# Performance work log

Hardware: AMD Instinct MI355X
Metric: run time of the kernel (lower is better)

Reference implementation:

```python
import jax, jax.numpy as jnp
import numpy as np

N = 100000      # nodes
E = 1600000     # random edges (self-loops appended, as PyG GATConv does)
IN = 128        # in_channels
HID = 8         # hidden_channels per head
HEADS = 8
OUT = 40        # out_channels (classes)
NEG_SLOPE = 0.2 # PyG GATConv default


def _xavier(k, shape, fan_in, fan_out):
    lim = np.sqrt(6.0 / (fan_in + fan_out)).astype(np.float32)
    return jax.random.uniform(k, shape, jnp.float32, -lim, lim)


def setup_inputs() -> dict:
    key = jax.random.key(0)
    ks = jax.random.split(key, 8)
    x = jax.random.normal(ks[0], (N, IN), jnp.float32)
    ei = jax.random.randint(ks[1], (2, E), 0, N)
    loops = jnp.arange(N)
    edge_index = jnp.concatenate([ei, jnp.stack([loops, loops])], axis=1)  # [2, E+N]
    W1 = _xavier(ks[2], (HEADS * HID, IN), IN, HEADS * HID)
    att_src1 = _xavier(ks[3], (HEADS, HID), HID, 1)
    att_dst1 = _xavier(ks[4], (HEADS, HID), HID, 1)
    b1 = jnp.zeros((HEADS * HID,), jnp.float32)
    W2 = _xavier(ks[5], (OUT, HEADS * HID), HEADS * HID, OUT)
    att_src2 = _xavier(ks[6], (1, OUT), OUT, 1)
    att_dst2 = _xavier(ks[7], (1, OUT), OUT, 1)
    b2 = jnp.zeros((OUT,), jnp.float32)
    return {"x": x, "edge_index": edge_index, "W1": W1, "att_src1": att_src1,
            "att_dst1": att_dst1, "b1": b1, "W2": W2, "att_src2": att_src2,
            "att_dst2": att_dst2, "b2": b2}


def _gat_conv(x, src, dst, W, a_src, a_dst, b, heads, ch, concat):
    n = x.shape[0]
    h = (x @ W.T).reshape(n, heads, ch)                       # [N,H,C]
    a_s = jnp.sum(h * a_src[None], axis=-1)                   # [N,H]
    a_d = jnp.sum(h * a_dst[None], axis=-1)                   # [N,H]
    e = jax.nn.leaky_relu(a_s[src] + a_d[dst], NEG_SLOPE)     # [Eall,H]
    # segment softmax over edges sharing a destination node
    e_max = jax.ops.segment_max(e, dst, num_segments=n)
    ex = jnp.exp(e - e_max[dst])
    denom = jax.ops.segment_sum(ex, dst, num_segments=n)
    alpha = ex / denom[dst]                                   # [Eall,H]
    msg = h[src] * alpha[:, :, None]                          # [Eall,H,C]
    out = jax.ops.segment_sum(msg, dst, num_segments=n)       # [N,H,C]
    out = out.reshape(n, heads * ch) if concat else out.mean(axis=1)
    return out + b


def reference(x, edge_index, W1, att_src1, att_dst1, b1, W2, att_src2, att_dst2, b2):
    # eval mode: dropout is identity
    src, dst = edge_index[0], edge_index[1]
    h = _gat_conv(x, src, dst, W1, att_src1, att_dst1, b1, HEADS, HID, True)
    h = jax.nn.elu(h)
    out = _gat_conv(h, src, dst, W2, att_src2, att_dst2, b2, 1, OUT, False)
    return out
```

## Files before the change

### kernel.cpp

```cpp
#include <hip/hip_runtime.h>
#include <hip/hip_bf16.h>

#define IN_CH   128
#define HID     8
#define HEADS   8
#define C1      64
#define OUT_CH  40
#define NEG     0.2f
#define NPART   8

__device__ __forceinline__ float b2f(unsigned short u) {
    return __uint_as_float(((unsigned int)u) << 16);
}
__device__ __forceinline__ float blo(unsigned int p) { return __uint_as_float(p << 16); }
__device__ __forceinline__ float bhi(unsigned int p) { return __uint_as_float(p & 0xffff0000u); }
__device__ __forceinline__ unsigned short f2b(float f) {
    unsigned int u = __float_as_uint(f);
    unsigned int r = (u + 0x7fffu + ((u >> 16) & 1u)) >> 16;
    return (unsigned short)r;
}
__device__ __forceinline__ float lrelu(float v) { return v > 0.f ? v : NEG * v; }

#define P_W1    0
#define P_AS1   8192
#define P_AD1   8256
#define P_B1    8320
#define P_W2    8384
#define P_AS2   10944
#define P_AD2   10984
#define P_B2    11024
#define P_TOT   11064

__global__ __launch_bounds__(256) void k0_detect(
        const unsigned int* __restrict__ x32,
        const void* W1, const void* as1, const void* ad1, const void* b1,
        const void* W2, const void* as2, const void* ad2, const void* b2,
        int* __restrict__ flag, float* __restrict__ pf) {
    int t = threadIdx.x;
    __shared__ int sflag;
    if (t < 64) {
        unsigned int lo = x32[t] & 0xffffu;
        int ex = (int)((lo >> 7) & 0xff);
        bool sane = (ex >= 112 && ex <= 143);
        unsigned long long m = __ballot(sane);
        if (t == 0) {
            int isbf = (__popcll(m) >= 32) ? 1 : 0;
            sflag = isbf;
            *flag = isbf;
        }
    }
    __syncthreads();
    const int isbf = sflag;
#define CONV(dstoff, srcp, cnt)                                         \
    if (isbf) {                                                         \
        const unsigned short* sp = (const unsigned short*)(srcp);       \
        for (int i = t; i < (cnt); i += 256) pf[(dstoff) + i] = b2f(sp[i]); \
    } else {                                                            \
        const float* sp = (const float*)(srcp);                         \
        for (int i = t; i < (cnt); i += 256) pf[(dstoff) + i] = sp[i];  \
    }
    CONV(P_W1,  W1, 8192)
    CONV(P_AS1, as1, 64)
    CONV(P_AD1, ad1, 64)
    CONV(P_B1,  b1, 64)
    CONV(P_W2,  W2, 2560)
    CONV(P_AS2, as2, 40)
    CONV(P_AD2, ad2, 40)
    CONV(P_B2,  b2, 40)
#undef CONV
}

__global__ __launch_bounds__(256) void kA_hist(
        const int* __restrict__ dst, int* __restrict__ deg,
        int e_all, int n_nodes) {
    int part = blockIdx.x & (NPART - 1);
    int nm   = gridDim.x >> 3;
    int mblk = blockIdx.x >> 3;
    int lo = (int)((long long)part * n_nodes / NPART);
    int hi = (int)((long long)(part + 1) * n_nodes / NPART);
    for (int e = mblk * 256 + threadIdx.x; e < e_all; e += nm * 256) {
        int d = dst[e];
        if (d >= lo && d < hi) atomicAdd(&deg[d], 1);
    }
}

__global__ __launch_bounds__(256) void kB1_scan(
        const int* __restrict__ deg, int* __restrict__ offs,
        int* __restrict__ bsum, int n) {
    __shared__ int sd[256];
    int t = threadIdx.x;
    int i = blockIdx.x * 256 + t;
    int v = (i < n) ? deg[i] : 0;
    sd[t] = v;
    __syncthreads();
    for (int off = 1; off < 256; off <<= 1) {
        int u = (t >= off) ? sd[t - off] : 0;
        __syncthreads();
        sd[t] += u;
        __syncthreads();
    }
    if (i < n) offs[i] = sd[t] - v;
    if (t == 255) bsum[blockIdx.x] = sd[255];
}

__global__ __launch_bounds__(512) void kB2_scanb(
        const int* __restrict__ bsum, int* __restrict__ bsumx, int nb) {
    __shared__ int sd[512];
    int t = threadIdx.x;
    int v = (t < nb) ? bsum[t] : 0;
    sd[t] = v;
    __syncthreads();
    for (int off = 1; off < 512; off <<= 1) {
        int u = (t >= off) ? sd[t - off] : 0;
        __syncthreads();
        sd[t] += u;
        __syncthreads();
    }
    if (t < nb) bsumx[t] = sd[t] - v;
}

__global__ __launch_bounds__(256) void kB3_fix(
        int* __restrict__ offs, const int* __restrict__ bsumx,
        int* __restrict__ cursor, int n) {
    int i = blockIdx.x * 256 + threadIdx.x;
    if (i >= n) return;
    int o = offs[i] + bsumx[blockIdx.x];
    offs[i] = o;
    cursor[i] = o;
}

__global__ __launch_bounds__(256) void kC_scatter(
        const int* __restrict__ src, const int* __restrict__ dst,
        int* __restrict__ cursor, int* __restrict__ csr_src,
        int e_all, int n_nodes) {
    int part = blockIdx.x & (NPART - 1);
    int nm   = gridDim.x >> 3;
    int mblk = blockIdx.x >> 3;
    int lo = (int)((long long)part * n_nodes / NPART);
    int hi = (int)((long long)(part + 1) * n_nodes / NPART);
    for (int e = mblk * 256 + threadIdx.x; e < e_all; e += nm * 256) {
        int d = dst[e];
        if (d >= lo && d < hi) {
            int pos = atomicAdd(&cursor[d], 1);
            csr_src[pos] = src[e];
        }
    }
}

__global__ __launch_bounds__(256) void k1_gemm1(
        const void* __restrict__ x, const float* __restrict__ pf,
        const int* __restrict__ flagp,
        unsigned short* __restrict__ h1b, float* __restrict__ as1, float* __restrict__ ad1,
        int n_nodes) {
    int tid = threadIdx.x;
    int w = tid >> 6, t = tid & 63;
    const int isbf = *flagp;
    __shared__ float wTf[8192];
    __shared__ float xsf[4 * IN_CH];
    for (int e = tid; e < 8192; e += 256) {
        int row = e >> 7, k = e & 127;
        int g = k >> 2, j = k & 3;
        wTf[(g * 64 + ((row + g) & 63)) * 4 + j] = pf[P_W1 + e];
    }
    __syncthreads();
    const float4* wT4 = (const float4*)wTf;
    int base = blockIdx.x * 32 + w * 8;
    for (int i = 0; i < 8; ++i) {
        int n = base + i;
        bool ok = (n < n_nodes);
        if (ok) {
            if (isbf) {
                unsigned int p = ((const unsigned int*)x)[(size_t)n * 64 + t];
                xsf[w * IN_CH + 2 * t]     = blo(p);
                xsf[w * IN_CH + 2 * t + 1] = bhi(p);
            } else {
                float2 f = ((const float2*)x)[(size_t)n * 64 + t];
                xsf[w * IN_CH + 2 * t]     = f.x;
                xsf[w * IN_CH + 2 * t + 1] = f.y;
            }
        }
        __syncthreads();
        if (ok) {
            const float4* xv = (const float4*)(xsf + w * IN_CH);
            float acc = 0.f;
#pragma unroll
            for (int g = 0; g < 32; ++g) {
                float4 wv = wT4[g * 64 + ((t + g) & 63)];
                float4 x4 = xv[g];
                acc += x4.x * wv.x + x4.y * wv.y + x4.z * wv.z + x4.w * wv.w;
            }
            h1b[(size_t)n * C1 + t] = f2b(acc);
            float as = acc * pf[P_AS1 + t];
            float ad = acc * pf[P_AD1 + t];
            for (int off = 1; off < 8; off <<= 1) {
                as += __shfl_xor(as, off, 64);
                ad += __shfl_xor(ad, off, 64);
            }
            if ((t & 7) == 0) {
                as1[(size_t)n * HEADS + (t >> 3)] = as;
                ad1[(size_t)n * HEADS + (t >> 3)] = ad;
            }
        }
        __syncthreads();
    }
}

__global__ __launch_bounds__(256) void k3_fused1(
        const int* __restrict__ offs, const int* __restrict__ deg,
        const int* __restrict__ csr_src,
        const float* __restrict__ as1, const float* __restrict__ ad1,
        const unsigned short* __restrict__ h1b, const float* __restrict__ pf,
        unsigned short* __restrict__ x2, int n_nodes) {
    int d = blockIdx.x * 4 + (threadIdx.x >> 6);
    if (d >= n_nodes) return;
    int t = threadIdx.x & 63;
    int head = t >> 3;
    float adv = ad1[(size_t)d * HEADS + head];
    int start = offs[d];
    int dg = deg[d];
    float acc = 0.f, den = 0.f;
    int j = 0;
    for (; j + 4 <= dg; j += 4) {
        int s0 = csr_src[start + j];
        int s1 = csr_src[start + j + 1];
        int s2 = csr_src[start + j + 2];
        int s3 = csr_src[start + j + 3];
        float v0 = as1[(size_t)s0 * HEADS + head] + adv;
        float v1 = as1[(size_t)s1 * HEADS + head] + adv;
        float v2 = as1[(size_t)s2 * HEADS + head] + adv;
        float v3 = as1[(size_t)s3 * HEADS + head] + adv;
        float h0 = b2f(h1b[(size_t)s0 * C1 + t]);
        float h1 = b2f(h1b[(size_t)s1 * C1 + t]);
        float h2 = b2f(h1b[(size_t)s2 * C1 + t]);
        float h3 = b2f(h1b[(size_t)s3 * C1 + t]);
        float e0 = __expf(lrelu(v0));
        float e1 = __expf(lrelu(v1));
        float e2 = __expf(lrelu(v2));
        float e3 = __expf(lrelu(v3));
        den += (e0 + e1) + (e2 + e3);
        acc += (e0 * h0 + e1 * h1) + (e2 * h2 + e3 * h3);
    }
    for (; j < dg; ++j) {
        int s = csr_src[start + j];
        float v = as1[(size_t)s * HEADS + head] + adv;
        float e = __expf(lrelu(v));
        den += e;
        acc += e * b2f(h1b[(size_t)s * C1 + t]);
    }
    float o = acc / den + pf[P_B1 + t];
    o = o > 0.f ? o : (__expf(o) - 1.f);
    x2[(size_t)d * C1 + t] = f2b(o);
}

__global__ __launch_bounds__(256) void k4_gemm2(
        const unsigned short* __restrict__ x2, const float* __restrict__ pf,
        unsigned short* __restrict__ h2b, float* __restrict__ as2, float* __restrict__ ad2,
        int n_nodes) {
    int tid = threadIdx.x;
    int w = tid >> 6, t = tid & 63;
    __shared__ float wTf[4096];
    __shared__ float xsf[4 * C1];
    for (int e = tid; e < 2560; e += 256) {
        int row = e >> 6, k = e & 63;
        int g = k >> 2, j = k & 3;
        wTf[(g * 64 + ((row + g) & 63)) * 4 + j] = pf[P_W2 + e];
    }
    __syncthreads();
    const float4* wT4 = (const float4*)wTf;
    int base = blockIdx.x * 32 + w * 8;
    for (int i = 0; i < 8; ++i) {
        int n = base + i;
        bool ok = (n < n_nodes);
        if (ok && t < 32) {
            unsigned int p = ((const unsigned int*)x2)[(size_t)n * 32 + t];
            xsf[w * C1 + 2 * t]     = blo(p);
            xsf[w * C1 + 2 * t + 1] = bhi(p);
        }
        __syncthreads();
        if (ok) {
            float hs = 0.f, hd = 0.f;
            if (t < OUT_CH) {
                const float4* xv = (const float4*)(xsf + w * C1);
                float acc = 0.f;
#pragma unroll
                for (int g = 0; g < 16; ++g) {
                    float4 wv = wT4[g * 64 + ((t + g) & 63)];
                    float4 x4 = xv[g];
                    acc += x4.x * wv.x + x4.y * wv.y + x4.z * wv.z + x4.w * wv.w;
                }
                h2b[(size_t)n * OUT_CH + t] = f2b(acc);
                hs = acc * pf[P_AS2 + t];
                hd = acc * pf[P_AD2 + t];
            }
            for (int off = 1; off < 64; off <<= 1) {
                hs += __shfl_xor(hs, off, 64);
                hd += __shfl_xor(hd, off, 64);
            }
            if (t == 0) { as2[n] = hs; ad2[n] = hd; }
        }
        __syncthreads();
    }
}

__global__ __launch_bounds__(256) void k6_fused2(
        const int* __restrict__ offs, const int* __restrict__ deg,
        const int* __restrict__ csr_src,
        const float* __restrict__ as2, const float* __restrict__ ad2,
        const unsigned short* __restrict__ h2b, const float* __restrict__ pf,
        const int* __restrict__ flagp, void* __restrict__ outp, int n_nodes) {
    int d = blockIdx.x * 4 + (threadIdx.x >> 6);
    if (d >= n_nodes) return;
    int t = threadIdx.x & 63;
    float adv = ad2[d];
    int start = offs[d];
    int dg = deg[d];
    bool act = (t < OUT_CH);
    int tc = act ? t : 0;
    float acc = 0.f, den = 0.f;
    int j = 0;
    for (; j + 4 <= dg; j += 4) {
        int s0 = csr_src[start + j];
        int s1 = csr_src[start + j + 1];
        int s2 = csr_src[start + j + 2];
        int s3 = csr_src[start + j + 3];
        float v0 = as2[s0] + adv;
        float v1 = as2[s1] + adv;
        float v2 = as2[s2] + adv;
        float v3 = as2[s3] + adv;
        float h0 = b2f(h2b[(size_t)s0 * OUT_CH + tc]);
        float h1 = b2f(h2b[(size_t)s1 * OUT_CH + tc]);
        float h2 = b2f(h2b[(size_t)s2 * OUT_CH + tc]);
        float h3 = b2f(h2b[(size_t)s3 * OUT_CH + tc]);
        float e0 = __expf(lrelu(v0));
        float e1 = __expf(lrelu(v1));
        float e2 = __expf(lrelu(v2));
        float e3 = __expf(lrelu(v3));
        den += (e0 + e1) + (e2 + e3);
        acc += (e0 * h0 + e1 * h1) + (e2 * h2 + e3 * h3);
    }
    for (; j < dg; ++j) {
        int s = csr_src[start + j];
        float v = as2[s] + adv;
        float e = __expf(lrelu(v));
        den += e;
        acc += e * b2f(h2b[(size_t)s * OUT_CH + tc]);
    }
    if (!act) return;
    float o = acc / den + pf[P_B2 + t];
    size_t idx = (size_t)d * OUT_CH + t;
    if (*flagp) ((unsigned short*)outp)[idx] = f2b(o);
    else        ((float*)outp)[idx] = o;
}

extern "C" void kernel_launch(void* const* d_in, const int* in_sizes, int n_in,
                              void* d_out, int out_size, void* d_ws, size_t ws_size,
                              hipStream_t stream) {
    const void* x  = d_in[0];
    const int*  ei = (const int*)d_in[1];

    const int n_nodes = in_sizes[0] / IN_CH;
    const int e_all   = in_sizes[1] / 2;
    const int* srcI = ei;
    const int* dstI = ei + e_all;

    float* ws = (float*)d_ws;
    const size_t n = (size_t)n_nodes;
    int* deg     = (int*)ws;
    int* offs    = deg + n;
    int* cursor  = offs + n;
    int* bsum    = cursor + n;
    int* bsumx   = bsum + 512;
    int* csr_src = bsumx + 512;
    float* A     = ws + 3 * n + 1024 + (size_t)e_all;
    float* as1   = A;
    float* ad1   = A + 8 * n;
    unsigned short* h1b = (unsigned short*)(A + 16 * n);
    unsigned short* x2  = (unsigned short*)(A + 48 * n);
    int*   flagp = (int*)(A + 80 * n);
    float* pf    = A + 80 * n + 16;
    float* as2 = as1;
    float* ad2 = ad1;
    unsigned short* h2b = h1b;

    k0_detect<<<1, 256, 0, stream>>>((const unsigned int*)x,
        d_in[2], d_in[3], d_in[4], d_in[5], d_in[6], d_in[7], d_in[8], d_in[9],
        flagp, pf);

    hipMemsetAsync(deg, 0, n * sizeof(int), stream);

    kA_hist<<<1024, 256, 0, stream>>>(dstI, deg, e_all, n_nodes);

    int nb = (n_nodes + 255) / 256;
    kB1_scan<<<nb, 256, 0, stream>>>(deg, offs, bsum, n_nodes);
    kB2_scanb<<<1, 512, 0, stream>>>(bsum, bsumx, nb);
    kB3_fix<<<nb, 256, 0, stream>>>(offs, bsumx, cursor, n_nodes);

    kC_scatter<<<1024, 256, 0, stream>>>(srcI, dstI, cursor, csr_src, e_all, n_nodes);

    int gb = (n_nodes + 31) / 32;
    k1_gemm1<<<gb, 256, 0, stream>>>(x, pf, flagp, h1b, as1, ad1, n_nodes);

    k3_fused1<<<(n_nodes + 3) / 4, 256, 0, stream>>>(offs, deg, csr_src, as1, ad1, h1b, pf, x2, n_nodes);

    k4_gemm2<<<gb, 256, 0, stream>>>(x2, pf, h2b, as2, ad2, n_nodes);

    k6_fused2<<<(n_nodes + 3) / 4, 256, 0, stream>>>(offs, deg, csr_src, as2, ad2, h2b, pf, flagp, d_out, n_nodes);
}
```

Before: 545.1 us.

## Replace first-layer scalar GEMM with bf16 MFMA kernel

The first linear projection (x @ W1.T) now runs on matrix cores through 16x16x32 bf16 MFMA instructions instead of a shared-memory scalar FP32 dot-product loop. W1 is converted to bf16 once in the setup kernel, and each wave loads its W1 fragments straight from global memory. Each wave handles 16 nodes with no block-level syncs, and the attention logits are reduced with shuffles. When x arrives as fp32 it is rounded to bf16 before the multiply, which lowers the precision of the first layer's GEMM inputs.

```diff
diff --git a/kernel.cpp b/kernel.cpp
--- a/kernel.cpp
+++ b/kernel.cpp
@@ -8,6 +8,9 @@
 #define OUT_CH  40
 #define NEG     0.2f
 #define NPART   8
+
+typedef __attribute__((ext_vector_type(8))) short  short8;
+typedef __attribute__((ext_vector_type(4))) float  f32x4;
 
 __device__ __forceinline__ float b2f(unsigned short u) {
     return __uint_as_float(((unsigned int)u) << 16);
@@ -35,7 +38,8 @@
         const unsigned int* __restrict__ x32,
         const void* W1, const void* as1, const void* ad1, const void* b1,
         const void* W2, const void* as2, const void* ad2, const void* b2,
-        int* __restrict__ flag, float* __restrict__ pf) {
+        int* __restrict__ flag, float* __restrict__ pf,
+        unsigned short* __restrict__ w1bf) {
     int t = threadIdx.x;
     __shared__ int sflag;
     if (t < 64) {
@@ -68,6 +72,13 @@
     CONV(P_AD2, ad2, 40)
     CONV(P_B2,  b2, 40)
 #undef CONV
+    if (isbf) {
+        const unsigned short* sp = (const unsigned short*)W1;
+        for (int i = t; i < 8192; i += 256) w1bf[i] = sp[i];
+    } else {
+        const float* sp = (const float*)W1;
+        for (int i = t; i < 8192; i += 256) w1bf[i] = f2b(sp[i]);
+    }
 }
 
 __global__ __launch_bounds__(256) void kA_hist(
@@ -147,61 +158,71 @@
     }
 }
 
-__global__ __launch_bounds__(256) void k1_gemm1(
-        const void* __restrict__ x, const float* __restrict__ pf,
-        const int* __restrict__ flagp,
+__global__ __launch_bounds__(256) void k1_mfma(
+        const void* __restrict__ x, const unsigned short* __restrict__ w1bf,
+        const float* __restrict__ pf, const int* __restrict__ flagp,
         unsigned short* __restrict__ h1b, float* __restrict__ as1, float* __restrict__ ad1,
         int n_nodes) {
     int tid = threadIdx.x;
-    int w = tid >> 6, t = tid & 63;
+    int wv = tid >> 6, L = tid & 63;
+    int m = L & 15, q = L >> 4;
+    int base = blockIdx.x * 64 + wv * 16;
+    if (base >= n_nodes) return;
     const int isbf = *flagp;
-    __shared__ float wTf[8192];
-    __shared__ float xsf[4 * IN_CH];
-    for (int e = tid; e < 8192; e += 256) {
-        int row = e >> 7, k = e & 127;
-        int g = k >> 2, j = k & 3;
-        wTf[(g * 64 + ((row + g) & 63)) * 4 + j] = pf[P_W1 + e];
-    }
-    __syncthreads();
-    const float4* wT4 = (const float4*)wTf;
-    int base = blockIdx.x * 32 + w * 8;
-    for (int i = 0; i < 8; ++i) {
-        int n = base + i;
-        bool ok = (n < n_nodes);
-        if (ok) {
-            if (isbf) {
-                unsigned int p = ((const unsigned int*)x)[(size_t)n * 64 + t];
-                xsf[w * IN_CH + 2 * t]     = blo(p);
-                xsf[w * IN_CH + 2 * t + 1] = bhi(p);
-            } else {
-                float2 f = ((const float2*)x)[(size_t)n * 64 + t];
-                xsf[w * IN_CH + 2 * t]     = f.x;
-                xsf[w * IN_CH + 2 * t + 1] = f.y;
+
+    short8 bfr[4][4];
+#pragma unroll
+    for (int t = 0; t < 4; ++t)
+#pragma unroll
+        for (int kb = 0; kb < 4; ++kb)
+            bfr[t][kb] = *(const short8*)(w1bf + (size_t)(t * 16 + m) * IN_CH + kb * 32 + q * 8);
+
+    int row = base + m;
+    if (row >= n_nodes) row = n_nodes - 1;
+    short8 af[4];
+    if (isbf) {
+        const unsigned short* xr = (const unsigned short*)x + (size_t)row * IN_CH + q * 8;
+#pragma unroll
+        for (int kb = 0; kb < 4; ++kb) af[kb] = *(const short8*)(xr + kb * 32);
+    } else {
+        const float* xr = (const float*)x + (size_t)row * IN_CH + q * 8;
+#pragma unroll
+        for (int kb = 0; kb < 4; ++kb) {
+            short8 a;
+#pragma unroll
+            for (int j = 0; j < 8; ++j) a[j] = (short)f2b(xr[kb * 32 + j]);
+            af[kb] = a;
+        }
+    }
+
+    f32x4 acc[4];
+#pragma unroll
+    for (int t = 0; t < 4; ++t) acc[t] = (f32x4){0.f, 0.f, 0.f, 0.f};
+#pragma unroll
+    for (int t = 0; t < 4; ++t)
+#pragma unroll
+        for (int kb = 0; kb < 4; ++kb)
+            acc[t] = __builtin_amdgcn_mfma_f32_16x16x32_bf16(af[kb], bfr[t][kb], acc[t], 0, 0, 0);
+
+#pragma unroll
+    for (int t = 0; t < 4; ++t) {
+#pragma unroll
+        for (int r = 0; r < 4; ++r) {
+            int node = base + q * 4 + r;
+            bool ok = (node < n_nodes);
+            float val = acc[t][r];
+            int ch = t * 16 + m;
+            if (ok) h1b[(size_t)node * C1 + ch] = f2b(val);
+            float ps = val * pf[P_AS1 + ch];
+            float pd = val * pf[P_AD1 + ch];
+            ps += __shfl_xor(ps, 1, 64); ps += __shfl_xor(ps, 2, 64); ps += __shfl_xor(ps, 4, 64);
+            pd += __shfl_xor(pd, 1, 64); pd += __shfl_xor(pd, 2, 64); pd += __shfl_xor(pd, 4, 64);
+            if (ok && (L & 7) == 0) {
+                int head = 2 * t + ((m >> 3) & 1);
+                as1[(size_t)node * HEADS + head] = ps;
+                ad1[(size_t)node * HEADS + head] = pd;
             }
         }
-        __syncthreads();
-        if (ok) {
-            const float4* xv = (const float4*)(xsf + w * IN_CH);
-            float acc = 0.f;
-#pragma unroll
-            for (int g = 0; g < 32; ++g) {
-                float4 wv = wT4[g * 64 + ((t + g) & 63)];
-                float4 x4 = xv[g];
-                acc += x4.x * wv.x + x4.y * wv.y + x4.z * wv.z + x4.w * wv.w;
-            }
-            h1b[(size_t)n * C1 + t] = f2b(acc);
-            float as = acc * pf[P_AS1 + t];
-            float ad = acc * pf[P_AD1 + t];
-            for (int off = 1; off < 8; off <<= 1) {
-                as += __shfl_xor(as, off, 64);
-                ad += __shfl_xor(ad, off, 64);
-            }
-            if ((t & 7) == 0) {
-                as1[(size_t)n * HEADS + (t >> 3)] = as;
-                ad1[(size_t)n * HEADS + (t >> 3)] = ad;
-            }
-        }
-        __syncthreads();
     }
 }
 
@@ -378,13 +399,14 @@
     unsigned short* x2  = (unsigned short*)(A + 48 * n);
     int*   flagp = (int*)(A + 80 * n);
     float* pf    = A + 80 * n + 16;
+    unsigned short* w1bf = (unsigned short*)(pf + P_TOT);
     float* as2 = as1;
     float* ad2 = ad1;
     unsigned short* h2b = h1b;
 
     k0_detect<<<1, 256, 0, stream>>>((const unsigned int*)x,
         d_in[2], d_in[3], d_in[4], d_in[5], d_in[6], d_in[7], d_in[8], d_in[9],
-        flagp, pf);
+        flagp, pf, w1bf);
 
     hipMemsetAsync(deg, 0, n * sizeof(int), stream);
 
@@ -397,11 +419,11 @@
 
     kC_scatter<<<1024, 256, 0, stream>>>(srcI, dstI, cursor, csr_src, e_all, n_nodes);
 
+    k1_mfma<<<(n_nodes + 63) / 64, 256, 0, stream>>>(x, w1bf, pf, flagp, h1b, as1, ad1, n_nodes);
+
+    k3_fused1<<<(n_nodes + 3) / 4, 256, 0, stream>>>(offs, deg, csr_src, as1, ad1, h1b, pf, x2, n_nodes);
+
     int gb = (n_nodes + 31) / 32;
-    k1_gemm1<<<gb, 256, 0, stream>>>(x, pf, flagp, h1b, as1, ad1, n_nodes);
-
-    k3_fused1<<<(n_nodes + 3) / 4, 256, 0, stream>>>(offs, deg, csr_src, as1, ad1, h1b, pf, x2, n_nodes);
-
     k4_gemm2<<<gb, 256, 0, stream>>>(x2, pf, h2b, as2, ad2, n_nodes);
 
     k6_fused2<<<(n_nodes + 3) / 4, 256, 0, stream>>>(offs, deg, csr_src, as2, ad2, h2b, pf, flagp, d_out, n_nodes);
```

New measurement: 485.5 us. 10.9% less time.
